# Kernel optimization log

Measured on AMD Instinct MI355X. Metric: run time of the kernel, lower is better.

Reference implementation:

```python
import jax, jax.numpy as jnp
import numpy as np

HIDDEN_DIM = 1024
NUM_HEADS = 16
HEAD_DIM = HIDDEN_DIM // NUM_HEADS
SCALAR_NORM = float(np.sqrt(HIDDEN_DIM / NUM_HEADS))


def setup_inputs() -> dict:
    key = jax.random.key(0)
    k1, k2 = jax.random.split(key)
    B, N, D = 2, 2048, HIDDEN_DIM
    x = jax.random.normal(k1, (B, N, D), dtype=jnp.float32)
    # torch Linear weight shape: (3D, D); xavier_uniform-like scale
    limit = float(np.sqrt(6.0 / (D + 3 * D)))
    W_qkv = jax.random.uniform(k2, (3 * D, D), dtype=jnp.float32, minval=-limit, maxval=limit)
    return {"x": x, "W_qkv": W_qkv}


def reference(x, W_qkv):
    b, n, d = x.shape
    h, hd = NUM_HEADS, HEAD_DIM
    qkv = x @ W_qkv.T  # (B, N, 3D)
    q, k, v = jnp.split(qkv, 3, axis=-1)
    # (B, H, N, hd)
    q = q.reshape(b, n, h, hd).transpose(0, 2, 1, 3)
    k = k.reshape(b, n, h, hd).transpose(0, 2, 1, 3)
    v = v.reshape(b, n, h, hd).transpose(0, 2, 1, 3)
    scores = jnp.einsum('bhik,bhjk->bhij', q, k) / SCALAR_NORM
    attn = jax.nn.softmax(scores, axis=-1)
    out = jnp.einsum('bhij,bhjk->bhik', attn, v)
    return out.transpose(0, 2, 1, 3).reshape(b, n, d)
```

## Files before the change

### kernel.cpp

```cpp
#include <hip/hip_runtime.h>
#include <hip/hip_bf16.h>

#define SEQ 2048
#define DMODEL 1024
#define NHEADS 16
#define HD 64
#define BATCH 2

typedef short bf16x8 __attribute__((ext_vector_type(8)));
typedef float f32x4 __attribute__((ext_vector_type(4)));

static __device__ inline ushort f2bf(float f) {
    unsigned u = __float_as_uint(f);
    return (ushort)((u + 0x7fffu + ((u >> 16) & 1u)) >> 16);
}

static __device__ inline void async16(const ushort* g, ushort* l) {
    __builtin_amdgcn_global_load_lds((const __attribute__((address_space(1))) void*)g,
                                     (__attribute__((address_space(3))) void*)l, 16, 0, 0);
}

__global__ void cvt2(const float* __restrict__ a, ushort* __restrict__ da, int na,
                     const float* __restrict__ b, ushort* __restrict__ db, int nb) {
    long i = (long)(blockIdx.x * blockDim.x + threadIdx.x) * 4;
    const float* s; ushort* d;
    if (i < na) { s = a + i; d = da + i; }
    else { long j = i - na; if (j >= nb) return; s = b + j; d = db + j; }
    float4 v = *(const float4*)s;
    ushort4 o; o.x = f2bf(v.x); o.y = f2bf(v.y); o.z = f2bf(v.z); o.w = f2bf(v.w);
    *(ushort4*)d = o;
}

__global__ __launch_bounds__(256) void qkv_gemm(
        const ushort* __restrict__ X, const ushort* __restrict__ W,
        ushort* __restrict__ Qd, ushort* __restrict__ Kd, ushort* __restrict__ VTd) {
    __shared__ ushort sA[128 * 64];
    __shared__ ushort sB[128 * 64];
    const int t = threadIdx.x;
    const int lane = t & 63, l15 = lane & 15, quad = lane >> 4;
    const int w = t >> 6, wm = w >> 1, wn = w & 1;
    const int gm = blockIdx.x, gn = blockIdx.y;
    const int srow = t >> 3, scol = (t & 7) * 8;

    f32x4 acc[4][4] = {};

    for (int kt = 0; kt < 16; ++kt) {
        const int k0 = kt * 64;
        __syncthreads();
#pragma unroll
        for (int inst = 0; inst < 4; ++inst) {
            async16(&X[(gm * 128 + inst * 32 + srow) * 1024 + k0 + scol], &sA[inst * 2048 + t * 8]);
            async16(&W[(gn * 128 + inst * 32 + srow) * 1024 + k0 + scol], &sB[inst * 2048 + t * 8]);
        }
        __syncthreads();
#pragma unroll
        for (int ks = 0; ks < 2; ++ks) {
            const int kk = ks * 32 + quad * 8;
            bf16x8 af[4], bfr[4];
#pragma unroll
            for (int i = 0; i < 4; ++i) {
                af[i]  = *(const bf16x8*)&sA[(wm * 64 + i * 16 + l15) * 64 + kk];
                bfr[i] = *(const bf16x8*)&sB[(wn * 64 + i * 16 + l15) * 64 + kk];
            }
#pragma unroll
            for (int i = 0; i < 4; ++i)
#pragma unroll
                for (int j = 0; j < 4; ++j)
                    acc[i][j] = __builtin_amdgcn_mfma_f32_16x16x32_bf16(af[i], bfr[j], acc[i][j], 0, 0, 0);
        }
    }
    const float SCQ = 0.125f * 1.44269504f;
#pragma unroll
    for (int j = 0; j < 4; ++j) {
        const int c = gn * 128 + wn * 64 + j * 16 + l15;
        const int which = c >> 10;
        const int rem = c & 1023;
        const int h = rem >> 6, hd = rem & 63;
#pragma unroll
        for (int i = 0; i < 4; ++i) {
#pragma unroll
            for (int reg = 0; reg < 4; ++reg) {
                const int m = gm * 128 + wm * 64 + i * 16 + quad * 4 + reg;
                const int b = m >> 11, n = m & 2047;
                const float v = acc[i][j][reg];
                if (which == 0)      Qd[((b * NHEADS + h) * SEQ + n) * HD + hd] = f2bf(v * SCQ);
                else if (which == 1) Kd[((b * NHEADS + h) * SEQ + n) * HD + hd] = f2bf(v);
                else                 VTd[(((long)(b * NHEADS + h)) * HD + hd) * SEQ + n] = f2bf(v);
            }
        }
    }
}

__global__ __launch_bounds__(128, 2) void attn_kernel(
        const ushort* __restrict__ Q, const ushort* __restrict__ K,
        const ushort* __restrict__ VT, float* __restrict__ O) {
    __shared__ ushort sK[64][72];
    __shared__ ushort sVT[64][72];
    __shared__ ushort sP[64][72];
    const int t = threadIdx.x;
    const int lane = t & 63, l15 = lane & 15, quad = lane >> 4;
    const int w = t >> 6;
    const int qt = blockIdx.x, bh = blockIdx.y;
    const ushort* Qp = Q + ((long)bh * SEQ + qt * 64) * HD;
    const ushort* Kp = K + (long)bh * SEQ * HD;
    const ushort* Vp = VT + (long)bh * HD * SEQ;
    const int r0 = t >> 3, c8 = (t & 7) * 8;

    bf16x8 aq[2][2];
#pragma unroll
    for (int st = 0; st < 2; ++st)
#pragma unroll
        for (int kc = 0; kc < 2; ++kc)
            aq[st][kc] = *(const bf16x8*)&Qp[(w * 32 + st * 16 + l15) * HD + kc * 32 + quad * 8];

    f32x4 accO[2][4] = {};
    f32x4 accL[2] = {};
    bf16x8 ones;
#pragma unroll
    for (int j = 0; j < 8; ++j) ones[j] = (short)0x3F80;

    for (int kt = 0; kt < 32; ++kt) {
        __syncthreads();
#pragma unroll
        for (int rr = 0; rr < 64; rr += 16) {
            *(bf16x8*)&sK[rr + r0][c8]  = *(const bf16x8*)&Kp[(kt * 64 + rr + r0) * HD + c8];
            *(bf16x8*)&sVT[rr + r0][c8] = *(const bf16x8*)&Vp[(rr + r0) * SEQ + kt * 64 + c8];
        }
        __syncthreads();

        f32x4 s[2][4];
#pragma unroll
        for (int st = 0; st < 2; ++st)
#pragma unroll
            for (int nb = 0; nb < 4; ++nb) {
                f32x4 z = {};
                z = __builtin_amdgcn_mfma_f32_16x16x32_bf16(aq[st][0], *(const bf16x8*)&sK[nb * 16 + l15][quad * 8], z, 0, 0, 0);
                z = __builtin_amdgcn_mfma_f32_16x16x32_bf16(aq[st][1], *(const bf16x8*)&sK[nb * 16 + l15][32 + quad * 8], z, 0, 0, 0);
                s[st][nb] = z;
            }

#pragma unroll
        for (int st = 0; st < 2; ++st)
#pragma unroll
            for (int r = 0; r < 4; ++r) {
                const int row = w * 32 + st * 16 + quad * 4 + r;
#pragma unroll
                for (int nb = 0; nb < 4; ++nb)
                    sP[row][(nb * 16 + l15) ^ (quad << 4)] = f2bf(exp2f(s[st][nb][r]));
            }

        bf16x8 ap[2][2];
#pragma unroll
        for (int st = 0; st < 2; ++st)
#pragma unroll
            for (int kb = 0; kb < 2; ++kb)
                ap[st][kb] = *(const bf16x8*)&sP[w * 32 + st * 16 + l15][(kb * 32 + quad * 8) ^ ((l15 & 12) << 2)];

#pragma unroll
        for (int st = 0; st < 2; ++st) {
#pragma unroll
            for (int ob = 0; ob < 4; ++ob)
#pragma unroll
                for (int kb = 0; kb < 2; ++kb)
                    accO[st][ob] = __builtin_amdgcn_mfma_f32_16x16x32_bf16(
                        ap[st][kb], *(const bf16x8*)&sVT[ob * 16 + l15][kb * 32 + quad * 8], accO[st][ob], 0, 0, 0);
#pragma unroll
            for (int kb = 0; kb < 2; ++kb)
                accL[st] = __builtin_amdgcn_mfma_f32_16x16x32_bf16(ap[st][kb], ones, accL[st], 0, 0, 0);
        }
    }

    const int b = bh >> 4, h = bh & 15;
#pragma unroll
    for (int st = 0; st < 2; ++st)
#pragma unroll
        for (int r = 0; r < 4; ++r) {
            const float inv = 1.0f / accL[st][r];
            const int row = qt * 64 + w * 32 + st * 16 + quad * 4 + r;
#pragma unroll
            for (int ob = 0; ob < 4; ++ob)
                O[((long)b * SEQ + row) * DMODEL + h * HD + ob * 16 + l15] = accO[st][ob][r] * inv;
        }
}

extern "C" void kernel_launch(void* const* d_in, const int* in_sizes, int n_in,
                              void* d_out, int out_size, void* d_ws, size_t ws_size,
                              hipStream_t stream) {
    const float* x  = (const float*)d_in[0];
    const float* Wq = (const float*)d_in[1];
    float* out = (float*)d_out;

    const int NX = BATCH * SEQ * DMODEL;
    const int NW = 3 * DMODEL * DMODEL;
    const int NQKV = BATCH * NHEADS * SEQ * HD;

    ushort* xb = (ushort*)d_ws;
    ushort* wb = xb + NX;
    ushort* q  = wb + NW;
    ushort* k  = q + NQKV;
    ushort* vt = k + NQKV;

    cvt2<<<(NX + NW) / 4 / 256, 256, 0, stream>>>(x, xb, NX, Wq, wb, NW);

    dim3 g1(4096 / 128, 3072 / 128);
    qkv_gemm<<<g1, 256, 0, stream>>>(xb, wb, q, k, vt);

    dim3 g2(SEQ / 64, BATCH * NHEADS);
    attn_kernel<<<g2, 128, 0, stream>>>(q, k, vt, out);
}
```

Baseline: 199.4 us.

## Stage QKV GEMM epilogue through LDS for vectorized stores, transpose V separately

The GEMM epilogue now writes bf16 results into a swizzled shared-memory tile and then issues coalesced 16-byte stores in head-major layout. This replaces the scattered 2-byte global stores, which were especially poor for the transposed V. V is written row-major and a new small kernel transposes it into the xb workspace region, which is reused once the GEMM has finished. Packed float-to-bf16 conversion is also used in the GEMM epilogue and in the attention P writes. The cost is an extra kernel launch and an extra pass over V.

New measurement: 195.1 us. 2.2% less time.

```diff
diff --git a/kernel.cpp b/kernel.cpp
--- a/kernel.cpp
+++ b/kernel.cpp
@@ -13,6 +13,12 @@
 static __device__ inline ushort f2bf(float f) {
     unsigned u = __float_as_uint(f);
     return (ushort)((u + 0x7fffu + ((u >> 16) & 1u)) >> 16);
+}
+
+static __device__ inline unsigned pk2bf(float a, float b) {
+    __hip_bfloat162 h = __float22bfloat162_rn(make_float2(a, b));
+    union { __hip_bfloat162 h; unsigned u; } c; c.h = h;
+    return c.u;
 }
 
 static __device__ inline void async16(const ushort* g, ushort* l) {
@@ -31,11 +37,15 @@
     *(ushort4*)d = o;
 }
 
+union GemmSmem {
+    struct { ushort A[128 * 64]; ushort B[128 * 64]; } st;
+    ushort C[128 * 128];
+};
+
 __global__ __launch_bounds__(256) void qkv_gemm(
         const ushort* __restrict__ X, const ushort* __restrict__ W,
-        ushort* __restrict__ Qd, ushort* __restrict__ Kd, ushort* __restrict__ VTd) {
-    __shared__ ushort sA[128 * 64];
-    __shared__ ushort sB[128 * 64];
+        ushort* __restrict__ Qd, ushort* __restrict__ Kd, ushort* __restrict__ Vd) {
+    __shared__ GemmSmem sm;
     const int t = threadIdx.x;
     const int lane = t & 63, l15 = lane & 15, quad = lane >> 4;
     const int w = t >> 6, wm = w >> 1, wn = w & 1;
@@ -49,8 +59,8 @@
         __syncthreads();
 #pragma unroll
         for (int inst = 0; inst < 4; ++inst) {
-            async16(&X[(gm * 128 + inst * 32 + srow) * 1024 + k0 + scol], &sA[inst * 2048 + t * 8]);
-            async16(&W[(gn * 128 + inst * 32 + srow) * 1024 + k0 + scol], &sB[inst * 2048 + t * 8]);
+            async16(&X[(gm * 128 + inst * 32 + srow) * 1024 + k0 + scol], &sm.st.A[inst * 2048 + t * 8]);
+            async16(&W[(gn * 128 + inst * 32 + srow) * 1024 + k0 + scol], &sm.st.B[inst * 2048 + t * 8]);
         }
         __syncthreads();
 #pragma unroll
@@ -59,8 +69,8 @@
             bf16x8 af[4], bfr[4];
 #pragma unroll
             for (int i = 0; i < 4; ++i) {
-                af[i]  = *(const bf16x8*)&sA[(wm * 64 + i * 16 + l15) * 64 + kk];
-                bfr[i] = *(const bf16x8*)&sB[(wn * 64 + i * 16 + l15) * 64 + kk];
+                af[i]  = *(const bf16x8*)&sm.st.A[(wm * 64 + i * 16 + l15) * 64 + kk];
+                bfr[i] = *(const bf16x8*)&sm.st.B[(wn * 64 + i * 16 + l15) * 64 + kk];
             }
 #pragma unroll
             for (int i = 0; i < 4; ++i)
@@ -69,25 +79,57 @@
                     acc[i][j] = __builtin_amdgcn_mfma_f32_16x16x32_bf16(af[i], bfr[j], acc[i][j], 0, 0, 0);
         }
     }
-    const float SCQ = 0.125f * 1.44269504f;
-#pragma unroll
-    for (int j = 0; j < 4; ++j) {
-        const int c = gn * 128 + wn * 64 + j * 16 + l15;
-        const int which = c >> 10;
-        const int rem = c & 1023;
-        const int h = rem >> 6, hd = rem & 63;
-#pragma unroll
-        for (int i = 0; i < 4; ++i) {
-#pragma unroll
-            for (int reg = 0; reg < 4; ++reg) {
-                const int m = gm * 128 + wm * 64 + i * 16 + quad * 4 + reg;
-                const int b = m >> 11, n = m & 2047;
-                const float v = acc[i][j][reg];
-                if (which == 0)      Qd[((b * NHEADS + h) * SEQ + n) * HD + hd] = f2bf(v * SCQ);
-                else if (which == 1) Kd[((b * NHEADS + h) * SEQ + n) * HD + hd] = f2bf(v);
-                else                 VTd[(((long)(b * NHEADS + h)) * HD + hd) * SEQ + n] = f2bf(v);
-            }
-        }
+
+    __syncthreads();
+    const float sc = (gn < 8) ? (0.125f * 1.44269504f) : 1.0f;
+#pragma unroll
+    for (int i = 0; i < 4; ++i)
+#pragma unroll
+        for (int reg = 0; reg < 4; ++reg) {
+            const int row = wm * 64 + i * 16 + quad * 4 + reg;
+            const int sw = (row & 7) * 8;
+#pragma unroll
+            for (int jp = 0; jp < 4; jp += 2) {
+                unsigned u = pk2bf(acc[i][jp][reg] * sc, acc[i][jp + 1][reg] * sc);
+                sm.C[row * 128 + ((wn * 64 + jp * 16 + l15) ^ sw)] = (ushort)u;
+                sm.C[row * 128 + ((wn * 64 + (jp + 1) * 16 + l15) ^ sw)] = (ushort)(u >> 16);
+            }
+        }
+    __syncthreads();
+
+    const int which = gn >> 3;
+    ushort* dst = (which == 0) ? Qd : ((which == 1) ? Kd : Vd);
+    const int rloc = t >> 4, l = t & 15;
+#pragma unroll
+    for (int pass = 0; pass < 8; ++pass) {
+        const int r = pass * 16 + rloc;
+        bf16x8 v = *(const bf16x8*)&sm.C[r * 128 + ((l * 8) ^ ((r & 7) * 8))];
+        const int ng = gm * 128 + r;
+        const int b = ng >> 11, n = ng & 2047;
+        const int cl = (gn * 128 + l * 8) & 1023;
+        const int h = cl >> 6, hd = cl & 63;
+        *(bf16x8*)&dst[(((b * NHEADS + h) * SEQ) + n) * HD + hd] = v;
+    }
+}
+
+__global__ __launch_bounds__(256) void tr_v(const ushort* __restrict__ src, ushort* __restrict__ dst) {
+    __shared__ ushort sT[64][72];
+    const int t = threadIdx.x;
+    const int bh = blockIdx.y, nt = blockIdx.x;
+    const int r0 = t >> 3, c8 = (t & 7) * 8;
+    const ushort* sp = src + ((long)bh * SEQ + nt * 64) * HD;
+#pragma unroll
+    for (int rr = 0; rr < 64; rr += 32)
+        *(bf16x8*)&sT[rr + r0][c8] = *(const bf16x8*)&sp[(rr + r0) * HD + c8];
+    __syncthreads();
+    ushort* dp = dst + (long)bh * HD * SEQ + nt * 64;
+#pragma unroll
+    for (int rr = 0; rr < 64; rr += 32) {
+        const int hd = rr + r0;
+        bf16x8 v;
+#pragma unroll
+        for (int j = 0; j < 8; ++j) v[j] = (short)sT[c8 + j][hd];
+        *(bf16x8*)&dp[(long)hd * SEQ + c8] = v;
     }
 }
 
@@ -145,8 +187,11 @@
             for (int r = 0; r < 4; ++r) {
                 const int row = w * 32 + st * 16 + quad * 4 + r;
 #pragma unroll
-                for (int nb = 0; nb < 4; ++nb)
-                    sP[row][(nb * 16 + l15) ^ (quad << 4)] = f2bf(exp2f(s[st][nb][r]));
+                for (int nb = 0; nb < 4; nb += 2) {
+                    unsigned u = pk2bf(exp2f(s[st][nb][r]), exp2f(s[st][nb + 1][r]));
+                    sP[row][(nb * 16 + l15) ^ (quad << 4)] = (ushort)u;
+                    sP[row][((nb + 1) * 16 + l15) ^ (quad << 4)] = (ushort)(u >> 16);
+                }
             }
 
         bf16x8 ap[2][2];
@@ -198,12 +243,16 @@
     ushort* wb = xb + NX;
     ushort* q  = wb + NW;
     ushort* k  = q + NQKV;
-    ushort* vt = k + NQKV;
+    ushort* vtmp = k + NQKV;
+    ushort* vt = xb;
 
     cvt2<<<(NX + NW) / 4 / 256, 256, 0, stream>>>(x, xb, NX, Wq, wb, NW);
 
     dim3 g1(4096 / 128, 3072 / 128);
-    qkv_gemm<<<g1, 256, 0, stream>>>(xb, wb, q, k, vt);
+    qkv_gemm<<<g1, 256, 0, stream>>>(xb, wb, q, k, vtmp);
+
+    dim3 gt(SEQ / 64, BATCH * NHEADS);
+    tr_v<<<gt, 256, 0, stream>>>(vtmp, vt);
 
     dim3 g2(SEQ / 64, BATCH * NHEADS);
     attn_kernel<<<g2, 128, 0, stream>>>(q, k, vt, out);
```
